# Kernel tuning notes

Hardware: AMD Instinct MI355X
Metric: run time of the kernel (lower is better)

Reference implementation:

```python
import jax, jax.numpy as jnp
import numpy as np

EMB = 1024
HID = 1536
NE = 8


def setup_inputs() -> dict:
    key = jax.random.key(0)
    ks = jax.random.split(key, 8)
    B, N, E, H, ne = 4, 2048, EMB, HID, NE
    s = 1.0 / np.sqrt(E)
    sh = 1.0 / np.sqrt(H)
    return {
        "x": jax.random.normal(ks[0], (B, N, E), dtype=jnp.float32),
        "Wr": jax.random.uniform(ks[1], (E, ne), minval=-s, maxval=s, dtype=jnp.float32),
        "br": jax.random.uniform(ks[2], (ne,), minval=-s, maxval=s, dtype=jnp.float32),
        "W1": jax.random.uniform(ks[3], (ne, E, H), minval=-s, maxval=s, dtype=jnp.float32),
        "b1": jax.random.uniform(ks[4], (ne, H), minval=-s, maxval=s, dtype=jnp.float32),
        "W2": jax.random.uniform(ks[5], (ne, H, E), minval=-sh, maxval=sh, dtype=jnp.float32),
        "b2": jax.random.uniform(ks[6], (ne, E), minval=-sh, maxval=sh, dtype=jnp.float32),
        "k": 2,
    }


def reference(x, Wr, br, W1, b1, W2, b2, k):
    B, N, E = x.shape
    T = B * N
    ne = Wr.shape[1]
    flat = x.reshape(T, E)
    logits = flat @ Wr + br                      # [T, ne]
    _, topk_idx = jax.lax.top_k(logits, k)       # [T, k]
    # counts[t, e] = number of top-k slots of token t assigned to expert e
    counts = jax.nn.one_hot(topk_idx, ne, dtype=flat.dtype).sum(axis=1)  # [T, ne]
    out = jnp.zeros_like(flat)
    for e in range(ne):  # small fixed loop over experts (structurally distinct weights)
        h = jax.nn.gelu(flat @ W1[e] + b1[e], approximate=False)  # torch nn.GELU = exact erf
        y = h @ W2[e] + b2[e]
        out = out + counts[:, e:e + 1] * y
    out = out / k
    return out.reshape(B, N, E)
```

## Files before the change

### kernel.cpp

```cpp
#include <hip/hip_runtime.h>
#include <hip/hip_bf16.h>
#include <math.h>

#define T_TOK 8192
#define EMB   1024
#define HID   1536
#define NE    8

typedef float  floatx4 __attribute__((ext_vector_type(4)));
typedef __bf16 bf16x8  __attribute__((ext_vector_type(8)));

#define WS_COUNTS   0
#define WS_OFFSETS  1024
#define WS_TOKMAP   8192
#define WS_TOKLIST  270336
#define WS_YBUF     532480
#define WS_W1T      34086912
#define WS_W2T      59252736
#define WS_H        84418560
#define WS_NEEDED   135143424

__device__ __forceinline__ bool wave_sniff_f32(const void* p, int nelem) {
  const unsigned* w = (const unsigned*)p;
  int nw = nelem >> 1; if (nw > 256) nw = 256;
  const int lane = threadIdx.x & 63;
  int pl = 0, nz = 0;
  for (int i = lane; i < nw; i += 64) {
    unsigned v = w[i];
    if (v) { nz++; unsigned ex = (v >> 23) & 255; if (ex >= 100 && ex <= 150) pl++; }
  }
#pragma unroll
  for (int off = 32; off; off >>= 1) { pl += __shfl_xor(pl, off, 64); nz += __shfl_xor(nz, off, 64); }
  return 2 * pl > nz;
}

__device__ __forceinline__ float eload(const void* p, size_t idx, bool f32) {
  return f32 ? ((const float*)p)[idx] : (float)(((const __bf16*)p)[idx]);
}

__device__ __forceinline__ void glds16(const void* g, void* l) {
  __builtin_amdgcn_global_load_lds(
      (const __attribute__((address_space(1))) unsigned int*)g,
      (__attribute__((address_space(3))) unsigned int*)l, 16, 0, 0);
}

__global__ __launch_bounds__(256)
void prep_kernel(const void* __restrict__ W1, const void* __restrict__ W2,
                 __bf16* __restrict__ w1t, __bf16* __restrict__ w2t,
                 const void* __restrict__ x, const void* __restrict__ Wr,
                 const void* __restrict__ br, const int* __restrict__ kptr,
                 int* __restrict__ tokmap, __bf16* __restrict__ xbf) {
  const int bid = blockIdx.x;
  const int tid = threadIdx.x;
  const int wave = tid >> 6;
  const int lane = tid & 63;

  if (bid < 1536) {
    const void* in; __bf16* out; int K, N; int t;
    if (bid < 768) {
      in = W1; out = w1t; K = EMB; N = HID;
      t = bid * 4 + wave;
    } else {
      in = W2; out = w2t; K = HID; N = EMB;
      t = (bid - 768) * 4 + wave;
    }
    const bool f32 = wave_sniff_f32(in, NE * EMB * HID);
    const int ntile = N / 64;
    const int e  = t / 384;
    const int r  = t % 384;
    const int kb = r / ntile;
    const int nb = r % ntile;
    const size_t eoff = (size_t)e * (size_t)K * (size_t)N;
    const int k0 = kb * 64 + (lane >> 3) * 8;
    const int n0 = nb * 64 + (lane & 7) * 8;

    if (f32) {
      floatx4 a0[8], a1[8];
#pragma unroll
      for (int i = 0; i < 8; ++i) {
        const float* g = (const float*)in + eoff + (size_t)(k0 + i) * N + n0;
        a0[i] = *(const floatx4*)g;
        a1[i] = *(const floatx4*)(g + 4);
      }
#pragma unroll
      for (int j = 0; j < 8; ++j) {
        bf16x8 o;
#pragma unroll
        for (int i = 0; i < 8; ++i)
          o[i] = (__bf16)(j < 4 ? a0[i][j] : a1[i][j - 4]);
        *(bf16x8*)(out + eoff + (size_t)(n0 + j) * K + k0) = o;
      }
    } else {
      bf16x8 a[8];
#pragma unroll
      for (int i = 0; i < 8; ++i)
        a[i] = *(const bf16x8*)((const __bf16*)in + eoff + (size_t)(k0 + i) * N + n0);
#pragma unroll
      for (int j = 0; j < 8; ++j) {
        bf16x8 o;
#pragma unroll
        for (int i = 0; i < 8; ++i) o[i] = a[i][j];
        *(bf16x8*)(out + eoff + (size_t)(n0 + j) * K + k0) = o;
      }
    }
    return;
  }

  const bool xf32  = wave_sniff_f32(x, T_TOK * EMB);
  const bool wrf32 = wave_sniff_f32(Wr, EMB * NE);
  const bool brf32 = wave_sniff_f32(br, NE);
  const int t = (bid - 1536) * 4 + wave;

  float xv[16];
  {
    size_t base = (size_t)t * EMB + lane * 16;
    if (xf32) {
      const float* g = (const float*)x + base;
#pragma unroll
      for (int c = 0; c < 4; ++c) {
        float4 v = *(const float4*)(g + c * 4);
        xv[c * 4 + 0] = v.x; xv[c * 4 + 1] = v.y; xv[c * 4 + 2] = v.z; xv[c * 4 + 3] = v.w;
      }
    } else {
      bf16x8 u = *(const bf16x8*)((const __bf16*)x + base);
      bf16x8 v = *(const bf16x8*)((const __bf16*)x + base + 8);
#pragma unroll
      for (int j = 0; j < 8; ++j) { xv[j] = (float)u[j]; xv[8 + j] = (float)v[j]; }
    }
  }
  {
    bf16x8 o0, o1;
#pragma unroll
    for (int j = 0; j < 8; ++j) { o0[j] = (__bf16)xv[j]; o1[j] = (__bf16)xv[8 + j]; }
    __bf16* xo = xbf + (size_t)t * EMB + lane * 16;
    *(bf16x8*)xo = o0;
    *(bf16x8*)(xo + 8) = o1;
  }
  float acc[NE];
#pragma unroll
  for (int e = 0; e < NE; ++e) acc[e] = 0.f;
  if (wrf32) {
#pragma unroll
    for (int j = 0; j < 16; ++j) {
      const float* wr = (const float*)Wr + (size_t)(lane * 16 + j) * NE;
#pragma unroll
      for (int e = 0; e < NE; ++e) acc[e] += xv[j] * wr[e];
    }
  } else {
#pragma unroll
    for (int j = 0; j < 16; ++j) {
      bf16x8 wr = *(const bf16x8*)((const __bf16*)Wr + (size_t)(lane * 16 + j) * NE);
#pragma unroll
      for (int e = 0; e < NE; ++e) acc[e] += xv[j] * (float)wr[e];
    }
  }
#pragma unroll
  for (int e = 0; e < NE; ++e) {
#pragma unroll
    for (int off = 32; off > 0; off >>= 1)
      acc[e] += __shfl_xor(acc[e], off, 64);
  }
  if (lane == 0) {
    int k = kptr[0];
    if (k < 1) k = 1; if (k > NE) k = NE;
    float lg[NE];
#pragma unroll
    for (int e = 0; e < NE; ++e) lg[e] = acc[e] + eload(br, e, brf32);
    for (int s = 0; s < k; ++s) {
      int bi = 0; float bv = lg[0];
#pragma unroll
      for (int e = 1; e < NE; ++e) { if (lg[e] > bv) { bv = lg[e]; bi = e; } }
      lg[bi] = -3.0e38f;
      tokmap[t * 8 + s] = bi;
    }
  }
}

__global__ __launch_bounds__(1024)
void bin_kernel(const int* __restrict__ kptr, int* __restrict__ tokmap,
                int* __restrict__ tok_list, int* __restrict__ counts,
                int* __restrict__ offsets) {
  __shared__ int lcnt[NE];
  __shared__ int soff[NE + 1];
  const int tid = threadIdx.x;
  if (tid < NE) lcnt[tid] = 0;
  __syncthreads();
  int k = kptr[0];
  if (k < 1) k = 1; if (k > NE) k = NE;
  for (int t = tid; t < T_TOK; t += 1024) {
    for (int s = 0; s < k; ++s) {
      int e = tokmap[t * 8 + s] & 7;
      int pos = atomicAdd(&lcnt[e], 1);
      tok_list[e * T_TOK + pos] = t;
      tokmap[t * 8 + s] = (e << 16) | pos;
    }
  }
  __syncthreads();
  if (tid == 0) {
    int s = 0;
    for (int e = 0; e < NE; ++e) { soff[e] = s; s += lcnt[e]; }
    soff[NE] = s;
  }
  __syncthreads();
  if (tid < NE) counts[tid] = lcnt[tid];
  if (tid <= NE) offsets[tid] = soff[tid];
  for (int e = 0; e < NE; ++e) {
    const int c = lcnt[e];
    const int end = (c + 127) & ~127;
    for (int i = c + tid; i < end; i += 1024) tok_list[e * T_TOK + i] = 0;
  }
}


__global__ __launch_bounds__(256, 4)
void gemm1_kernel(const __bf16* __restrict__ xbf, const __bf16* __restrict__ w1t,
                  const void* __restrict__ b1, const int* __restrict__ counts,
                  const int* __restrict__ offsets, const int* __restrict__ tok_list,
                  __bf16* __restrict__ hbuf) {
  const int flat = blockIdx.x;
  const int e   = flat & 7;
  const int idx = flat >> 3;
  const int g   = idx / 12;
  const int nT  = idx % 12;
  const int cnt = counts[e];
  const bool b1f32 = wave_sniff_f32(b1, NE * HID);

  __shared__ __align__(16) __bf16 As[128 * 64];
  __shared__ __align__(16) __bf16 Bs[128 * 64];

  const int wave = threadIdx.x >> 6;
  const int lane = threadIdx.x & 63;
  const int lrow = lane >> 3;
  const int cgs  = (lane & 7) ^ lrow;

  int Rst[4];
#pragma unroll
  for (int q = 0; q < 4; ++q) Rst[q] = (q * 4 + wave) * 8 + lrow;

  const __bf16* pB[4];
#pragma unroll
  for (int q = 0; q < 4; ++q)
    pB[q] = w1t + ((size_t)e * HID + nT * 128 + Rst[q]) * EMB + cgs * 8;

  const int wm = (wave & 1) * 64;
  const int wn = (wave >> 1) * 64;
  const int fr = lane & 15;
  const int fc = lane >> 4;
  int aOff0[4], aOff1[4], bOff0[4], bOff1[4];
#pragma unroll
  for (int i = 0; i < 4; ++i) {
    int R = wm + i * 16 + fr;
    aOff0[i] = R * 128 + (((fc)     ^ (R & 7)) << 4);
    aOff1[i] = R * 128 + (((fc + 4) ^ (R & 7)) << 4);
  }
#pragma unroll
  for (int j = 0; j < 4; ++j) {
    int R = wn + j * 16 + fr;
    bOff0[j] = R * 128 + (((fc)     ^ (R & 7)) << 4);
    bOff1[j] = R * 128 + (((fc + 4) ^ (R & 7)) << 4);
  }

  const int colBase = nT * 128 + wn + fr;
  float bv[4];
#pragma unroll
  for (int j = 0; j < 4; ++j) bv[j] = eload(b1, (size_t)e * HID + colBase + j * 16, b1f32);

  for (int mT = g; mT * 128 < cnt; mT += 16) {
    const __bf16* pA[4];
#pragma unroll
    for (int q = 0; q < 4; ++q) {
      const int tok = tok_list[e * T_TOK + mT * 128 + Rst[q]];
      pA[q] = xbf + (size_t)tok * EMB + cgs * 8;
    }

    floatx4 acc[4][4];
#pragma unroll
    for (int i = 0; i < 4; ++i)
#pragma unroll
      for (int j = 0; j < 4; ++j) acc[i][j] = (floatx4){0.f, 0.f, 0.f, 0.f};

    for (int kb = 0; kb < EMB / 64; ++kb) {
      __syncthreads();
#pragma unroll
      for (int q = 0; q < 4; ++q) glds16(pA[q] + (size_t)kb * 64, As + (q * 4 + wave) * 512);
#pragma unroll
      for (int q = 0; q < 4; ++q) glds16(pB[q] + (size_t)kb * 64, Bs + (q * 4 + wave) * 512);
      __syncthreads();
      bf16x8 af[4], bfr[4];
#pragma unroll
      for (int i = 0; i < 4; ++i) af[i]  = *(const bf16x8*)((const char*)As + aOff0[i]);
#pragma unroll
      for (int j = 0; j < 4; ++j) bfr[j] = *(const bf16x8*)((const char*)Bs + bOff0[j]);
#pragma unroll
      for (int i = 0; i < 4; ++i)
#pragma unroll
        for (int j = 0; j < 4; ++j)
          acc[i][j] = __builtin_amdgcn_mfma_f32_16x16x32_bf16(af[i], bfr[j], acc[i][j], 0, 0, 0);
#pragma unroll
      for (int i = 0; i < 4; ++i) af[i]  = *(const bf16x8*)((const char*)As + aOff1[i]);
#pragma unroll
      for (int j = 0; j < 4; ++j) bfr[j] = *(const bf16x8*)((const char*)Bs + bOff1[j]);
#pragma unroll
      for (int i = 0; i < 4; ++i)
#pragma unroll
        for (int j = 0; j < 4; ++j)
          acc[i][j] = __builtin_amdgcn_mfma_f32_16x16x32_bf16(af[i], bfr[j], acc[i][j], 0, 0, 0);
    }

    const int hBase = offsets[e] + mT * 128;
#pragma unroll
    for (int i = 0; i < 4; ++i) {
      const int rowLoc = wm + i * 16 + fc * 4;
#pragma unroll
      for (int r = 0; r < 4; ++r) {
        const int row = rowLoc + r;
        if (mT * 128 + row < cnt) {
          __bf16* hp = hbuf + (size_t)(hBase + row) * HID + colBase;
#pragma unroll
          for (int j = 0; j < 4; ++j) {
            float v = acc[i][j][r] + bv[j];
            float gl = 0.5f * v * (1.0f + erff(v * 0.70710678118654752f));
            hp[j * 16] = (__bf16)gl;
          }
        }
      }
    }
  }
}

__global__ __launch_bounds__(256, 4)
void gemm2_kernel(const __bf16* __restrict__ hbuf, const __bf16* __restrict__ w2t,
                  const void* __restrict__ b2, const int* __restrict__ counts,
                  const int* __restrict__ offsets, __bf16* __restrict__ ybuf) {
  const int flat = blockIdx.x;
  const int e   = flat & 7;
  const int idx = flat >> 3;
  const int g   = idx >> 3;
  const int nT  = idx & 7;
  const int cnt = counts[e];
  const bool b2f32 = wave_sniff_f32(b2, NE * EMB);

  __shared__ __align__(16) __bf16 As[128 * 64];
  __shared__ __align__(16) __bf16 Bs[128 * 64];

  const int wave = threadIdx.x >> 6;
  const int lane = threadIdx.x & 63;
  const int lrow = lane >> 3;
  const int cgs  = (lane & 7) ^ lrow;

  int Rst[4];
#pragma unroll
  for (int q = 0; q < 4; ++q) Rst[q] = (q * 4 + wave) * 8 + lrow;

  const __bf16* pB[4];
#pragma unroll
  for (int q = 0; q < 4; ++q)
    pB[q] = w2t + ((size_t)e * EMB + nT * 128 + Rst[q]) * HID + cgs * 8;

  const int wm = (wave & 1) * 64;
  const int wn = (wave >> 1) * 64;
  const int fr = lane & 15;
  const int fc = lane >> 4;
  int aOff0[4], aOff1[4], bOff0[4], bOff1[4];
#pragma unroll
  for (int i = 0; i < 4; ++i) {
    int R = wm + i * 16 + fr;
    aOff0[i] = R * 128 + (((fc)     ^ (R & 7)) << 4);
    aOff1[i] = R * 128 + (((fc + 4) ^ (R & 7)) << 4);
  }
#pragma unroll
  for (int j = 0; j < 4; ++j) {
    int R = wn + j * 16 + fr;
    bOff0[j] = R * 128 + (((fc)     ^ (R & 7)) << 4);
    bOff1[j] = R * 128 + (((fc + 4) ^ (R & 7)) << 4);
  }

  const int colBase = nT * 128 + wn + fr;
  float bv[4];
#pragma unroll
  for (int j = 0; j < 4; ++j) bv[j] = eload(b2, (size_t)e * EMB + colBase + j * 16, b2f32);

  for (int mT = g; mT * 128 < cnt; mT += 16) {
    const int rowBase = offsets[e] + mT * 128;
    const __bf16* pA[4];
#pragma unroll
    for (int q = 0; q < 4; ++q)
      pA[q] = hbuf + (size_t)(rowBase + Rst[q]) * HID + cgs * 8;

    floatx4 acc[4][4];
#pragma unroll
    for (int i = 0; i < 4; ++i)
#pragma unroll
      for (int j = 0; j < 4; ++j) acc[i][j] = (floatx4){0.f, 0.f, 0.f, 0.f};

    for (int kb = 0; kb < HID / 64; ++kb) {
      __syncthreads();
#pragma unroll
      for (int q = 0; q < 4; ++q) glds16(pA[q] + (size_t)kb * 64, As + (q * 4 + wave) * 512);
#pragma unroll
      for (int q = 0; q < 4; ++q) glds16(pB[q] + (size_t)kb * 64, Bs + (q * 4 + wave) * 512);
      __syncthreads();
      bf16x8 af[4], bfr[4];
#pragma unroll
      for (int i = 0; i < 4; ++i) af[i]  = *(const bf16x8*)((const char*)As + aOff0[i]);
#pragma unroll
      for (int j = 0; j < 4; ++j) bfr[j] = *(const bf16x8*)((const char*)Bs + bOff0[j]);
#pragma unroll
      for (int i = 0; i < 4; ++i)
#pragma unroll
        for (int j = 0; j < 4; ++j)
          acc[i][j] = __builtin_amdgcn_mfma_f32_16x16x32_bf16(af[i], bfr[j], acc[i][j], 0, 0, 0);
#pragma unroll
      for (int i = 0; i < 4; ++i) af[i]  = *(const bf16x8*)((const char*)As + aOff1[i]);
#pragma unroll
      for (int j = 0; j < 4; ++j) bfr[j] = *(const bf16x8*)((const char*)Bs + bOff1[j]);
#pragma unroll
      for (int i = 0; i < 4; ++i)
#pragma unroll
        for (int j = 0; j < 4; ++j)
          acc[i][j] = __builtin_amdgcn_mfma_f32_16x16x32_bf16(af[i], bfr[j], acc[i][j], 0, 0, 0);
    }

#pragma unroll
    for (int i = 0; i < 4; ++i) {
      const int rowLoc = wm + i * 16 + fc * 4;
#pragma unroll
      for (int r = 0; r < 4; ++r) {
        const int row = rowLoc + r;
        if (mT * 128 + row < cnt) {
          __bf16* yp = ybuf + (size_t)(rowBase + row) * EMB + colBase;
#pragma unroll
          for (int j = 0; j < 4; ++j)
            yp[j * 16] = (__bf16)(acc[i][j][r] + bv[j]);
        }
      }
    }
  }
}

__global__ __launch_bounds__(256)
void combine_kernel(const __bf16* __restrict__ ybuf, const int* __restrict__ tokmap,
                    const int* __restrict__ offsets, const int* __restrict__ kptr,
                    const void* __restrict__ x, void* __restrict__ out) {
  const bool f32 = wave_sniff_f32(x, T_TOK * EMB);
  const int wave = threadIdx.x >> 6;
  const int lane = threadIdx.x & 63;
  const int t = blockIdx.x * 4 + wave;
  int k = kptr[0];
  if (k < 1) k = 1; if (k > NE) k = NE;
  const float invk = 1.0f / (float)k;
  int rows[NE];
  for (int s = 0; s < k; ++s) {
    int m = tokmap[t * 8 + s];
    rows[s] = offsets[(m >> 16) & 7] + (m & 0xFFFF);
  }
#pragma unroll
  for (int c = 0; c < 2; ++c) {
    const int i = c * 512 + lane * 8;
    float a[8];
#pragma unroll
    for (int j = 0; j < 8; ++j) a[j] = 0.f;
    for (int s = 0; s < k; ++s) {
      bf16x8 y = *(const bf16x8*)(ybuf + (size_t)rows[s] * EMB + i);
#pragma unroll
      for (int j = 0; j < 8; ++j) a[j] += (float)y[j];
    }
    if (f32) {
      float* op = (float*)out + (size_t)t * EMB + i;
      float4 u = {a[0] * invk, a[1] * invk, a[2] * invk, a[3] * invk};
      float4 v = {a[4] * invk, a[5] * invk, a[6] * invk, a[7] * invk};
      *(float4*)op = u;
      *(float4*)(op + 4) = v;
    } else {
      bf16x8 o;
#pragma unroll
      for (int j = 0; j < 8; ++j) o[j] = (__bf16)(a[j] * invk);
      *(bf16x8*)((__bf16*)out + (size_t)t * EMB + i) = o;
    }
  }
}

extern "C" void kernel_launch(void* const* d_in, const int* in_sizes, int n_in,
                              void* d_out, int out_size, void* d_ws, size_t ws_size,
                              hipStream_t stream) {
  (void)in_sizes; (void)n_in; (void)out_size;
  if (ws_size < (size_t)WS_NEEDED) return;

  const void* x  = d_in[0];
  const void* Wr = d_in[1];
  const void* br = d_in[2];
  const void* W1 = d_in[3];
  const void* b1 = d_in[4];
  const void* W2 = d_in[5];
  const void* b2 = d_in[6];
  const int* kptr = (const int*)d_in[7];

  char* ws = (char*)d_ws;
  int*    counts   = (int*)(ws + WS_COUNTS);
  int*    offsets  = (int*)(ws + WS_OFFSETS);
  int*    tokmap   = (int*)(ws + WS_TOKMAP);
  int*    tok_list = (int*)(ws + WS_TOKLIST);
  __bf16* ybuf     = (__bf16*)(ws + WS_YBUF);
  __bf16* xbf      = (__bf16*)(ws + WS_YBUF);
  __bf16* w1t      = (__bf16*)(ws + WS_W1T);
  __bf16* w2t      = (__bf16*)(ws + WS_W2T);
  __bf16* hbuf     = (__bf16*)(ws + WS_H);

  prep_kernel<<<dim3(1536 + T_TOK / 4), 256, 0, stream>>>(
      W1, W2, w1t, w2t, x, Wr, br, kptr, tokmap, xbf);

  bin_kernel<<<dim3(1), 1024, 0, stream>>>(kptr, tokmap, tok_list, counts, offsets);

  gemm1_kernel<<<dim3(8 * 16 * 12), 256, 0, stream>>>(
      xbf, w1t, b1, counts, offsets, tok_list, hbuf);
  gemm2_kernel<<<dim3(8 * 16 * 8), 256, 0, stream>>>(
      hbuf, w2t, b2, counts, offsets, ybuf);

  combine_kernel<<<dim3(T_TOK / 4), 256, 0, stream>>>(ybuf, tokmap, offsets, kptr, x, d_out);
}
```

Measured before the change: 378.4 us.

## Move W2 transpose from prep kernel into gemm1 launch to overlap with GEMM

The W2 weight transpose/bf16 conversion is removed from the prep kernel and done by 768 extra blocks prepended to the gemm1 grid. Those blocks run alongside the first GEMM's tiles, so the W2 conversion overlaps with gemm1 compute instead of sitting on the critical path before binning. The cost is that gemm1's early blocks are spent on memory-bound transpose work, which can compete for bandwidth and delay GEMM tiles.

```diff
diff --git a/kernel.cpp b/kernel.cpp
--- a/kernel.cpp
+++ b/kernel.cpp
@@ -44,9 +44,51 @@
       (__attribute__((address_space(3))) unsigned int*)l, 16, 0, 0);
 }
 
+__device__ __forceinline__ void transpose_tile(const void* in, __bf16* out,
+                                               int K, int N, bool f32,
+                                               int t, int lane) {
+  const int ntile = N / 64;
+  const int e  = t / 384;
+  const int r  = t % 384;
+  const int kb = r / ntile;
+  const int nb = r % ntile;
+  const size_t eoff = (size_t)e * (size_t)K * (size_t)N;
+  const int k0 = kb * 64 + (lane >> 3) * 8;
+  const int n0 = nb * 64 + (lane & 7) * 8;
+
+  if (f32) {
+    floatx4 a0[8], a1[8];
+#pragma unroll
+    for (int i = 0; i < 8; ++i) {
+      const float* g = (const float*)in + eoff + (size_t)(k0 + i) * N + n0;
+      a0[i] = *(const floatx4*)g;
+      a1[i] = *(const floatx4*)(g + 4);
+    }
+#pragma unroll
+    for (int j = 0; j < 8; ++j) {
+      bf16x8 o;
+#pragma unroll
+      for (int i = 0; i < 8; ++i)
+        o[i] = (__bf16)(j < 4 ? a0[i][j] : a1[i][j - 4]);
+      *(bf16x8*)(out + eoff + (size_t)(n0 + j) * K + k0) = o;
+    }
+  } else {
+    bf16x8 a[8];
+#pragma unroll
+    for (int i = 0; i < 8; ++i)
+      a[i] = *(const bf16x8*)((const __bf16*)in + eoff + (size_t)(k0 + i) * N + n0);
+#pragma unroll
+    for (int j = 0; j < 8; ++j) {
+      bf16x8 o;
+#pragma unroll
+      for (int i = 0; i < 8; ++i) o[i] = a[i][j];
+      *(bf16x8*)(out + eoff + (size_t)(n0 + j) * K + k0) = o;
+    }
+  }
+}
+
 __global__ __launch_bounds__(256)
-void prep_kernel(const void* __restrict__ W1, const void* __restrict__ W2,
-                 __bf16* __restrict__ w1t, __bf16* __restrict__ w2t,
+void prep_kernel(const void* __restrict__ W1, __bf16* __restrict__ w1t,
                  const void* __restrict__ x, const void* __restrict__ Wr,
                  const void* __restrict__ br, const int* __restrict__ kptr,
                  int* __restrict__ tokmap, __bf16* __restrict__ xbf) {
@@ -55,61 +97,16 @@
   const int wave = tid >> 6;
   const int lane = tid & 63;
 
-  if (bid < 1536) {
-    const void* in; __bf16* out; int K, N; int t;
-    if (bid < 768) {
-      in = W1; out = w1t; K = EMB; N = HID;
-      t = bid * 4 + wave;
-    } else {
-      in = W2; out = w2t; K = HID; N = EMB;
-      t = (bid - 768) * 4 + wave;
-    }
-    const bool f32 = wave_sniff_f32(in, NE * EMB * HID);
-    const int ntile = N / 64;
-    const int e  = t / 384;
-    const int r  = t % 384;
-    const int kb = r / ntile;
-    const int nb = r % ntile;
-    const size_t eoff = (size_t)e * (size_t)K * (size_t)N;
-    const int k0 = kb * 64 + (lane >> 3) * 8;
-    const int n0 = nb * 64 + (lane & 7) * 8;
-
-    if (f32) {
-      floatx4 a0[8], a1[8];
-#pragma unroll
-      for (int i = 0; i < 8; ++i) {
-        const float* g = (const float*)in + eoff + (size_t)(k0 + i) * N + n0;
-        a0[i] = *(const floatx4*)g;
-        a1[i] = *(const floatx4*)(g + 4);
-      }
-#pragma unroll
-      for (int j = 0; j < 8; ++j) {
-        bf16x8 o;
-#pragma unroll
-        for (int i = 0; i < 8; ++i)
-          o[i] = (__bf16)(j < 4 ? a0[i][j] : a1[i][j - 4]);
-        *(bf16x8*)(out + eoff + (size_t)(n0 + j) * K + k0) = o;
-      }
-    } else {
-      bf16x8 a[8];
-#pragma unroll
-      for (int i = 0; i < 8; ++i)
-        a[i] = *(const bf16x8*)((const __bf16*)in + eoff + (size_t)(k0 + i) * N + n0);
-#pragma unroll
-      for (int j = 0; j < 8; ++j) {
-        bf16x8 o;
-#pragma unroll
-        for (int i = 0; i < 8; ++i) o[i] = a[i][j];
-        *(bf16x8*)(out + eoff + (size_t)(n0 + j) * K + k0) = o;
-      }
-    }
+  if (bid < 768) {
+    const bool f32 = wave_sniff_f32(W1, NE * EMB * HID);
+    transpose_tile(W1, w1t, EMB, HID, f32, bid * 4 + wave, lane);
     return;
   }
 
   const bool xf32  = wave_sniff_f32(x, T_TOK * EMB);
   const bool wrf32 = wave_sniff_f32(Wr, EMB * NE);
   const bool brf32 = wave_sniff_f32(br, NE);
-  const int t = (bid - 1536) * 4 + wave;
+  const int t = (bid - 768) * 4 + wave;
 
   float xv[16];
   {
@@ -211,13 +208,22 @@
   }
 }
 
-
 __global__ __launch_bounds__(256, 4)
 void gemm1_kernel(const __bf16* __restrict__ xbf, const __bf16* __restrict__ w1t,
                   const void* __restrict__ b1, const int* __restrict__ counts,
                   const int* __restrict__ offsets, const int* __restrict__ tok_list,
-                  __bf16* __restrict__ hbuf) {
-  const int flat = blockIdx.x;
+                  __bf16* __restrict__ hbuf,
+                  const void* __restrict__ W2, __bf16* __restrict__ w2t) {
+  const int bid = blockIdx.x;
+  const int lane = threadIdx.x & 63;
+
+  if (bid < 768) {
+    const bool f32 = wave_sniff_f32(W2, NE * EMB * HID);
+    transpose_tile(W2, w2t, HID, EMB, f32, bid * 4 + (threadIdx.x >> 6), lane);
+    return;
+  }
+
+  const int flat = bid - 768;
   const int e   = flat & 7;
   const int idx = flat >> 3;
   const int g   = idx / 12;
@@ -229,7 +235,6 @@
   __shared__ __align__(16) __bf16 Bs[128 * 64];
 
   const int wave = threadIdx.x >> 6;
-  const int lane = threadIdx.x & 63;
   const int lrow = lane >> 3;
   const int cgs  = (lane & 7) ^ lrow;
 
@@ -506,13 +511,14 @@
   __bf16* w2t      = (__bf16*)(ws + WS_W2T);
   __bf16* hbuf     = (__bf16*)(ws + WS_H);
 
-  prep_kernel<<<dim3(1536 + T_TOK / 4), 256, 0, stream>>>(
-      W1, W2, w1t, w2t, x, Wr, br, kptr, tokmap, xbf);
+  prep_kernel<<<dim3(768 + T_TOK / 4), 256, 0, stream>>>(
+      W1, w1t, x, Wr, br, kptr, tokmap, xbf);
 
   bin_kernel<<<dim3(1), 1024, 0, stream>>>(kptr, tokmap, tok_list, counts, offsets);
 
-  gemm1_kernel<<<dim3(8 * 16 * 12), 256, 0, stream>>>(
-      xbf, w1t, b1, counts, offsets, tok_list, hbuf);
+  gemm1_kernel<<<dim3(768 + 8 * 16 * 12), 256, 0, stream>>>(
+      xbf, w1t, b1, counts, offsets, tok_list, hbuf, W2, w2t);
+
   gemm2_kernel<<<dim3(8 * 16 * 8), 256, 0, stream>>>(
       hbuf, w2t, b2, counts, offsets, ybuf);
 
```

Result: no change. 372.4 us (median of 2 runs) (-1.6%).
